# Optimization experiments

Hardware: AMD Instinct MI355X
Metric: run time of the kernel (lower is better)

The kernel has to match this reference:

```python
import jax, jax.numpy as jnp
import numpy as np

NUM_AGENTS = 4
ACTOR_DIM = 128
OBS_DIM = 64
ACTION_SIZE = 16
BATCH = 65536


def _linear_params(key, din, dout):
    kw, kb = jax.random.split(key)
    bound = 1.0 / np.sqrt(din)
    W = jax.random.uniform(kw, (din, dout), jnp.float32, -bound, bound)
    b = jax.random.uniform(kb, (dout,), jnp.float32, -bound, bound)
    return W, b


def setup_inputs() -> dict:
    key = jax.random.key(0)
    ks = jax.random.split(key, 8)
    O = jax.random.normal(ks[0], (BATCH, NUM_AGENTS, OBS_DIM), jnp.float32)
    enc_w, enc_b = _linear_params(ks[1], OBS_DIM, ACTOR_DIM)
    fc1_w, fc1_b = _linear_params(ks[2], ACTOR_DIM, ACTOR_DIM)
    fc2_w, fc2_b = _linear_params(ks[3], ACTOR_DIM, ACTOR_DIM)
    fc3_w, fc3_b = _linear_params(ks[4], ACTOR_DIM, ACTOR_DIM)
    cl4_w, cl4_b = _linear_params(ks[5], 2 * ACTOR_DIM, ACTOR_DIM)
    dec_w, dec_b = _linear_params(ks[6], NUM_AGENTS * ACTOR_DIM, ACTION_SIZE)
    return {
        "O": O,
        "enc_w": enc_w, "enc_b": enc_b,
        "fc1_w": fc1_w, "fc1_b": fc1_b,
        "fc2_w": fc2_w, "fc2_b": fc2_b,
        "fc3_w": fc3_w, "fc3_b": fc3_b,
        "cl4_w": cl4_w, "cl4_b": cl4_b,
        "dec_w": dec_w, "dec_b": dec_b,
    }


def reference(O, enc_w, enc_b, fc1_w, fc1_b, fc2_w, fc2_b, fc3_w, fc3_b,
              cl4_w, cl4_b, dec_w, dec_b):
    # Encoding: sigmoid(Linear(obs)) -> [B, A, D]
    H0 = jax.nn.sigmoid(O @ enc_w + enc_b)
    H1 = jax.nn.relu(H0 @ fc1_w + fc1_b)
    H2 = jax.nn.relu(H1 @ fc2_w + fc2_b)
    H3 = jax.nn.relu(H2 @ fc3_w + fc3_b)
    # get_commvar: masked mean over OTHER agents, but torch divides by
    # num_agents (self slot is zeroed then included in the mean).
    # Equivalent fused form: C[b,i] = (sum_j H[b,j] - H[b,i]) / num_agents
    C = (jnp.sum(H3, axis=1, keepdims=True) - H3) / NUM_AGENTS
    H_cat = jnp.concatenate([H3, C], axis=-1)          # [B, A, 2D]
    H4 = H_cat @ cl4_w + cl4_b                          # [B, A, D] (no activation)
    H = H4.reshape(-1, NUM_AGENTS * ACTOR_DIM)          # [B, A*D]
    logits = H @ dec_w + dec_b                          # [B, action_size]
    return jax.nn.softmax(logits, axis=-1)
```

## Files before the change

### kernel.cpp

```cpp
#include <hip/hip_runtime.h>
#include <stdint.h>


typedef __attribute__((ext_vector_type(4)))  float f32x4;
typedef __attribute__((ext_vector_type(16))) float f32x16;
typedef __attribute__((ext_vector_type(8)))  _Float16 f16x8;
typedef __attribute__((ext_vector_type(4)))  _Float16 f16x4;

#define WS_HALF 106496
#define SEG_ENC 0
#define SEG_FC1 8192
#define SEG_FC2 24576
#define SEG_FC3 40960
#define SEG_W1  57344
#define SEG_W2  73728
#define SEG_DEC 90112

#define MFMA16(a, b, c) __builtin_amdgcn_mfma_f32_32x32x16_f16((a), (b), (c), 0, 0, 0)

__device__ __forceinline__ unsigned short f16_bits(float f) {
  union { _Float16 h; unsigned short u; } cv;
  cv.h = (_Float16)f;
  return cv.u;
}
__device__ __forceinline__ f32x16 zero16() {
  f32x16 v;
#pragma unroll
  for (int i = 0; i < 16; ++i) v[i] = 0.0f;
  return v;
}
__device__ __forceinline__ int xswz(int row, int g) {
  return row * 128 + ((g ^ (row & 15)) << 3);
}
__device__ __forceinline__ void barrier_lds() {
  asm volatile("s_waitcnt lgkmcnt(0)\n\ts_barrier" ::: "memory");
}

__global__ void prep_weights(const float* __restrict__ enc_w, const float* __restrict__ fc1_w,
                             const float* __restrict__ fc2_w, const float* __restrict__ fc3_w,
                             const float* __restrict__ cl4_w, const float* __restrict__ dec_w,
                             unsigned short* __restrict__ ws) {
  int idx = blockIdx.x * 256 + threadIdx.x;
  if (idx >= WS_HALF) return;
  const float* W; int base, N, nbN, mode;
  if      (idx <  8192) { W = enc_w; base = SEG_ENC; N = 128; nbN = 4; mode = 0; }
  else if (idx < 24576) { W = fc1_w; base = SEG_FC1; N = 128; nbN = 4; mode = 0; }
  else if (idx < 40960) { W = fc2_w; base = SEG_FC2; N = 128; nbN = 4; mode = 0; }
  else if (idx < 57344) { W = fc3_w; base = SEG_FC3; N = 128; nbN = 4; mode = 0; }
  else if (idx < 73728) { W = cl4_w; base = SEG_W1;  N = 128; nbN = 4; mode = 1; }
  else if (idx < 90112) { W = cl4_w; base = SEG_W2;  N = 128; nbN = 4; mode = 2; }
  else                  { W = dec_w; base = SEG_DEC; N = 16;  nbN = 1; mode = 0; }
  int local = idx - base;
  int j    = local & 7;
  int lane = (local >> 3) & 63;
  int frag = local >> 9;
  int nb = frag % nbN;
  int kc = frag / nbN;
  int k = kc * 16 + ((lane >> 5) << 3) + j;
  int n = nb * 32 + (lane & 31);
  float wv;
  if (mode == 0)      wv = (n < N) ? W[k * N + n] : 0.0f;
  else if (mode == 1) wv = W[k * 128 + n] - 0.25f * W[(k + 128) * 128 + n];
  else                wv = 0.25f * W[(k + 128) * 128 + n];
  ws[idx] = f16_bits(wv);
}

template <int KC, int ACT>
__device__ __forceinline__ void layer_std(short* __restrict__ Xh,
                                          const unsigned short* __restrict__ wseg,
                                          const float* __restrict__ bias,
                                          int lr, int lh, int w) {
  const int l = lh * 32 + lr;
  f32x16 acc0 = zero16(), acc1 = zero16();
  const unsigned short* bp = wseg + w * 512 + l * 8;
  f16x8 Bh[3];
  Bh[0] = *(const f16x8*)(bp);
  if (KC > 1) Bh[1] = *(const f16x8*)(bp + 2048);
  f32x4 bv[4];
#pragma unroll
  for (int q = 0; q < 4; ++q)
    bv[q] = *(const f32x4*)&bias[w * 32 + q * 8 + 4 * lh];
  barrier_lds();
#pragma unroll
  for (int kc = 0; kc < KC; ++kc) {
    const int cur = kc % 3;
    if (kc + 2 < KC) {
      Bh[(kc + 2) % 3] = *(const f16x8*)(bp + (kc + 2) * 2048);
    }
    const int g = kc * 2 + lh;
    const int xi0 = xswz(lr, g), xi1 = xswz(lr + 32, g);
    const f16x8 ah0 = *(const f16x8*)&Xh[xi0];
    const f16x8 ah1 = *(const f16x8*)&Xh[xi1];
    acc0 = MFMA16(Bh[cur], ah0, acc0);
    acc1 = MFMA16(Bh[cur], ah1, acc1);
  }
  barrier_lds();
#pragma unroll
  for (int mb = 0; mb < 2; ++mb) {
    const int row = mb * 32 + lr;
    const int rb = row & 15;
    const f32x16 a = mb ? acc1 : acc0;
#pragma unroll
    for (int q = 0; q < 4; ++q) {
      f16x4 hq;
#pragma unroll
      for (int t = 0; t < 4; ++t) {
        float v = a[q * 4 + t] + bv[q][t];
        if (ACT == 0)      v = __builtin_amdgcn_rcpf(1.0f + __expf(-v));
        else if (ACT == 1) v = fmaxf(v, 0.0f);
        hq[t] = (_Float16)v;
      }
      const int idx = row * 128 + (((w * 4 + q) ^ rb) << 3) + 4 * lh;
      *(f16x4*)&Xh[idx] = hq;
    }
  }
}

template <int MB>
__device__ __forceinline__ f32x16 cl4_band(const short* __restrict__ Xh,
                                           const unsigned short* __restrict__ ws,
                                           const float* __restrict__ cl4_b,
                                           int lr, int lh, int w) {
  const int l = lh * 32 + lr;
  f32x16 a1 = zero16(), a2 = zero16();
  const unsigned short* b1p = ws + SEG_W1 + w * 512 + l * 8;
  const unsigned short* b2p = ws + SEG_W2 + w * 512 + l * 8;
  f16x8 B1[2], B2[2];
  B1[0] = *(const f16x8*)(b1p);
  B2[0] = *(const f16x8*)(b2p);
  f32x4 bv[4];
#pragma unroll
  for (int q = 0; q < 4; ++q)
    bv[q] = *(const f32x4*)&cl4_b[w * 32 + q * 8 + 4 * lh];
#pragma unroll
  for (int kc = 0; kc < 8; ++kc) {
    const int cur = kc & 1;
    if (kc < 7) {
      const int nx = cur ^ 1;
      B1[nx] = *(const f16x8*)(b1p + (kc + 1) * 2048);
      B2[nx] = *(const f16x8*)(b2p + (kc + 1) * 2048);
    }
    const int xi = xswz(MB * 32 + lr, kc * 2 + lh);
    const f16x8 ah = *(const f16x8*)&Xh[xi];
    a1 = MFMA16(B1[cur], ah, a1);
    a2 = MFMA16(B2[cur], ah, a2);
  }
  f32x16 res;
#pragma unroll
  for (int r = 0; r < 16; ++r) {
    float t2 = a2[r];
    t2 += __shfl_xor(t2, 1);
    t2 += __shfl_xor(t2, 2);
    res[r] = a1[r] + t2 + bv[r >> 2][r & 3];
  }
  return res;
}

template <int MB>
__device__ __forceinline__ void cl4_write(short* __restrict__ Xh,
                                          const f32x16& rs, int lr, int lh, int w) {
  const int row = MB * 32 + lr;
  const int rb = row & 15;
#pragma unroll
  for (int q = 0; q < 4; ++q) {
    f16x4 hq;
#pragma unroll
    for (int t = 0; t < 4; ++t) hq[t] = (_Float16)rs[q * 4 + t];
    const int idx = row * 128 + (((w * 4 + q) ^ rb) << 3) + 4 * lh;
    *(f16x4*)&Xh[idx] = hq;
  }
}

__global__ __launch_bounds__(256, 4)
void commnet_fwd(const float* __restrict__ O,
                 const float* __restrict__ enc_b, const float* __restrict__ fc1_b,
                 const float* __restrict__ fc2_b, const float* __restrict__ fc3_b,
                 const float* __restrict__ cl4_b, const float* __restrict__ dec_b,
                 const unsigned short* __restrict__ ws, float* __restrict__ out) {
  __shared__ __attribute__((aligned(16))) short Xh[64 * 128];
  __shared__ __attribute__((aligned(16))) float Pbuf[272];

  const int tid = threadIdx.x;
  const int l = tid & 63, w = tid >> 6;
  const int lr = l & 31, lh = l >> 5;

  Pbuf[tid] = 0.0f;
  if (tid < 16) Pbuf[256 + tid] = 0.0f;

  {
    const f32x4* Og = (const f32x4*)(O + (long)blockIdx.x * 4096);
#pragma unroll
    for (int it = 0; it < 4; ++it) {
      const int i = it * 256 + tid;
      const int row = i >> 4;
      const int c4 = (i & 15) << 2;
      f32x4 v = Og[i];
      f16x4 hv;
#pragma unroll
      for (int j = 0; j < 4; ++j) hv[j] = (_Float16)v[j];
      const int bi = row * 128 + (((c4 >> 3) ^ (row & 15)) << 3) + (c4 & 7);
      *(f16x4*)&Xh[bi] = hv;
    }
  }

  layer_std<4, 0>(Xh, ws + SEG_ENC, enc_b, lr, lh, w);
  layer_std<8, 1>(Xh, ws + SEG_FC1, fc1_b, lr, lh, w);
  layer_std<8, 1>(Xh, ws + SEG_FC2, fc2_b, lr, lh, w);
  layer_std<8, 1>(Xh, ws + SEG_FC3, fc3_b, lr, lh, w);

  barrier_lds();
  {
    const f32x16 res0 = cl4_band<0>(Xh, ws, cl4_b, lr, lh, w);
    barrier_lds();
    cl4_write<0>(Xh, res0, lr, lh, w);
  }
  {
    const f32x16 res1 = cl4_band<1>(Xh, ws, cl4_b, lr, lh, w);
    barrier_lds();
    cl4_write<1>(Xh, res1, lr, lh, w);
  }
  barrier_lds();

  {
    f32x16 dacc = zero16();
    const unsigned short* bp = ws + SEG_DEC + (w * 8) * 512 + l * 8;
    f16x8 Bh[2];
    Bh[0] = *(const f16x8*)(bp);
#pragma unroll
    for (int kq = 0; kq < 8; ++kq) {
      const int cur = kq & 1;
      if (kq < 7) {
        Bh[cur ^ 1] = *(const f16x8*)(bp + (kq + 1) * 512);
      }
      const int kcg = w * 8 + kq;
      const int k0 = kcg * 16 + lh * 8;
      const int agent = k0 >> 7;
      const int d0 = k0 & 127;
      const int row = (lr & 15) * 4 + agent;
      const int xi = xswz(row, d0 >> 3);
      const f16x8 ah = *(const f16x8*)&Xh[xi];
      dacc = MFMA16(Bh[cur], ah, dacc);
    }
    if (lr < 16) {
#pragma unroll
      for (int r = 0; r < 8; ++r) {
        const int action = (r & 3) + 8 * (r >> 2) + 4 * lh;
        atomicAdd(&Pbuf[lr * 17 + action], dacc[r]);
      }
    }
  }
  barrier_lds();

  {
    const int c = tid & 15;
    float v = Pbuf[(tid >> 4) * 17 + c] + dec_b[c];
    float m = v;
#pragma unroll
    for (int mk = 1; mk < 16; mk <<= 1) m = fmaxf(m, __shfl_xor(m, mk, 16));
    const float e = __expf(v - m);
    float s = e;
#pragma unroll
    for (int mk = 1; mk < 16; mk <<= 1) s += __shfl_xor(s, mk, 16);
    out[(long)blockIdx.x * 256 + tid] = e * __builtin_amdgcn_rcpf(s);
  }
}

extern "C" void kernel_launch(void* const* d_in, const int* in_sizes, int n_in,
                              void* d_out, int out_size, void* d_ws, size_t ws_size,
                              hipStream_t stream) {
  (void)n_in; (void)out_size; (void)ws_size;
  const float* O     = (const float*)d_in[0];
  const float* enc_w = (const float*)d_in[1];
  const float* enc_b = (const float*)d_in[2];
  const float* fc1_w = (const float*)d_in[3];
  const float* fc1_b = (const float*)d_in[4];
  const float* fc2_w = (const float*)d_in[5];
  const float* fc2_b = (const float*)d_in[6];
  const float* fc3_w = (const float*)d_in[7];
  const float* fc3_b = (const float*)d_in[8];
  const float* cl4_w = (const float*)d_in[9];
  const float* cl4_b = (const float*)d_in[10];
  const float* dec_w = (const float*)d_in[11];
  const float* dec_b = (const float*)d_in[12];
  unsigned short* wsb = (unsigned short*)d_ws;

  prep_weights<<<(WS_HALF + 255) / 256, 256, 0, stream>>>(enc_w, fc1_w, fc2_w, fc3_w,
                                                          cl4_w, dec_w, wsb);
  const int rows   = in_sizes[0] / 64;
  const int blocks = rows / 64;
  commnet_fwd<<<blocks, 256, 0, stream>>>(O, enc_b, fc1_b, fc2_b, fc3_b, cl4_b,
                                          dec_b, wsb, (float*)d_out);
}
```

Baseline: 97.09 us.

## Ping-pong LDS activation buffers and prefetch all layer weights up front

Replaces the single in-place LDS activation tile with two ping-pong buffers. Each layer now needs one barrier instead of two, and the cl4 bands no longer need barriers between the compute and write-back steps. Weight fragments for each layer (and 4-deep for cl4, all 8 for the decoder) are loaded into registers before the MFMA loop, replacing the rolling 2-3 deep prefetch. The second buffer doubles LDS use to about 33 KB per block and raises VGPR pressure, which could cost occupancy against the launch bound of 4 blocks.

```diff
diff --git a/kernel.cpp b/kernel.cpp
--- a/kernel.cpp
+++ b/kernel.cpp
@@ -66,35 +66,30 @@
 }
 
 template <int KC, int ACT>
-__device__ __forceinline__ void layer_std(short* __restrict__ Xh,
+__device__ __forceinline__ void layer_std(const short* __restrict__ Xsrc,
+                                          short* __restrict__ Xdst,
                                           const unsigned short* __restrict__ wseg,
                                           const float* __restrict__ bias,
                                           int lr, int lh, int w) {
   const int l = lh * 32 + lr;
-  f32x16 acc0 = zero16(), acc1 = zero16();
   const unsigned short* bp = wseg + w * 512 + l * 8;
-  f16x8 Bh[3];
-  Bh[0] = *(const f16x8*)(bp);
-  if (KC > 1) Bh[1] = *(const f16x8*)(bp + 2048);
+  f16x8 Bh[KC];
+#pragma unroll
+  for (int kc = 0; kc < KC; ++kc) Bh[kc] = *(const f16x8*)(bp + kc * 2048);
   f32x4 bv[4];
 #pragma unroll
   for (int q = 0; q < 4; ++q)
     bv[q] = *(const f32x4*)&bias[w * 32 + q * 8 + 4 * lh];
-  barrier_lds();
+  f32x16 acc0 = zero16(), acc1 = zero16();
 #pragma unroll
   for (int kc = 0; kc < KC; ++kc) {
-    const int cur = kc % 3;
-    if (kc + 2 < KC) {
-      Bh[(kc + 2) % 3] = *(const f16x8*)(bp + (kc + 2) * 2048);
-    }
     const int g = kc * 2 + lh;
     const int xi0 = xswz(lr, g), xi1 = xswz(lr + 32, g);
-    const f16x8 ah0 = *(const f16x8*)&Xh[xi0];
-    const f16x8 ah1 = *(const f16x8*)&Xh[xi1];
-    acc0 = MFMA16(Bh[cur], ah0, acc0);
-    acc1 = MFMA16(Bh[cur], ah1, acc1);
-  }
-  barrier_lds();
+    const f16x8 ah0 = *(const f16x8*)&Xsrc[xi0];
+    const f16x8 ah1 = *(const f16x8*)&Xsrc[xi1];
+    acc0 = MFMA16(Bh[kc], ah0, acc0);
+    acc1 = MFMA16(Bh[kc], ah1, acc1);
+  }
 #pragma unroll
   for (int mb = 0; mb < 2; ++mb) {
     const int row = mb * 32 + lr;
@@ -111,63 +106,58 @@
         hq[t] = (_Float16)v;
       }
       const int idx = row * 128 + (((w * 4 + q) ^ rb) << 3) + 4 * lh;
-      *(f16x4*)&Xh[idx] = hq;
+      *(f16x4*)&Xdst[idx] = hq;
     }
   }
 }
 
 template <int MB>
-__device__ __forceinline__ f32x16 cl4_band(const short* __restrict__ Xh,
-                                           const unsigned short* __restrict__ ws,
-                                           const float* __restrict__ cl4_b,
-                                           int lr, int lh, int w) {
+__device__ __forceinline__ void cl4_band(const short* __restrict__ Xsrc,
+                                         short* __restrict__ Xdst,
+                                         const unsigned short* __restrict__ ws,
+                                         const float* __restrict__ cl4_b,
+                                         int lr, int lh, int w) {
   const int l = lh * 32 + lr;
-  f32x16 a1 = zero16(), a2 = zero16();
   const unsigned short* b1p = ws + SEG_W1 + w * 512 + l * 8;
   const unsigned short* b2p = ws + SEG_W2 + w * 512 + l * 8;
-  f16x8 B1[2], B2[2];
-  B1[0] = *(const f16x8*)(b1p);
-  B2[0] = *(const f16x8*)(b2p);
+  f16x8 B1[4], B2[4];
+#pragma unroll
+  for (int k = 0; k < 4; ++k) {
+    B1[k] = *(const f16x8*)(b1p + k * 2048);
+    B2[k] = *(const f16x8*)(b2p + k * 2048);
+  }
   f32x4 bv[4];
 #pragma unroll
   for (int q = 0; q < 4; ++q)
     bv[q] = *(const f32x4*)&cl4_b[w * 32 + q * 8 + 4 * lh];
+  f32x16 a1 = zero16(), a2 = zero16();
 #pragma unroll
   for (int kc = 0; kc < 8; ++kc) {
-    const int cur = kc & 1;
-    if (kc < 7) {
-      const int nx = cur ^ 1;
-      B1[nx] = *(const f16x8*)(b1p + (kc + 1) * 2048);
-      B2[nx] = *(const f16x8*)(b2p + (kc + 1) * 2048);
-    }
+    const int cur = kc & 3;
     const int xi = xswz(MB * 32 + lr, kc * 2 + lh);
-    const f16x8 ah = *(const f16x8*)&Xh[xi];
+    const f16x8 ah = *(const f16x8*)&Xsrc[xi];
     a1 = MFMA16(B1[cur], ah, a1);
     a2 = MFMA16(B2[cur], ah, a2);
-  }
-  f32x16 res;
-#pragma unroll
-  for (int r = 0; r < 16; ++r) {
-    float t2 = a2[r];
-    t2 += __shfl_xor(t2, 1);
-    t2 += __shfl_xor(t2, 2);
-    res[r] = a1[r] + t2 + bv[r >> 2][r & 3];
-  }
-  return res;
-}
-
-template <int MB>
-__device__ __forceinline__ void cl4_write(short* __restrict__ Xh,
-                                          const f32x16& rs, int lr, int lh, int w) {
+    if (kc + 4 < 8) {
+      B1[cur] = *(const f16x8*)(b1p + (kc + 4) * 2048);
+      B2[cur] = *(const f16x8*)(b2p + (kc + 4) * 2048);
+    }
+  }
   const int row = MB * 32 + lr;
   const int rb = row & 15;
 #pragma unroll
   for (int q = 0; q < 4; ++q) {
     f16x4 hq;
 #pragma unroll
-    for (int t = 0; t < 4; ++t) hq[t] = (_Float16)rs[q * 4 + t];
+    for (int t = 0; t < 4; ++t) {
+      const int r = q * 4 + t;
+      float t2 = a2[r];
+      t2 += __shfl_xor(t2, 1);
+      t2 += __shfl_xor(t2, 2);
+      hq[t] = (_Float16)(a1[r] + t2 + bv[q][t]);
+    }
     const int idx = row * 128 + (((w * 4 + q) ^ rb) << 3) + 4 * lh;
-    *(f16x4*)&Xh[idx] = hq;
+    *(f16x4*)&Xdst[idx] = hq;
   }
 }
 
@@ -177,7 +167,8 @@
                  const float* __restrict__ fc2_b, const float* __restrict__ fc3_b,
                  const float* __restrict__ cl4_b, const float* __restrict__ dec_b,
                  const unsigned short* __restrict__ ws, float* __restrict__ out) {
-  __shared__ __attribute__((aligned(16))) short Xh[64 * 128];
+  __shared__ __attribute__((aligned(16))) short X0[64 * 128];
+  __shared__ __attribute__((aligned(16))) short X1[64 * 128];
   __shared__ __attribute__((aligned(16))) float Pbuf[272];
 
   const int tid = threadIdx.x;
@@ -199,47 +190,40 @@
 #pragma unroll
       for (int j = 0; j < 4; ++j) hv[j] = (_Float16)v[j];
       const int bi = row * 128 + (((c4 >> 3) ^ (row & 15)) << 3) + (c4 & 7);
-      *(f16x4*)&Xh[bi] = hv;
-    }
-  }
-
-  layer_std<4, 0>(Xh, ws + SEG_ENC, enc_b, lr, lh, w);
-  layer_std<8, 1>(Xh, ws + SEG_FC1, fc1_b, lr, lh, w);
-  layer_std<8, 1>(Xh, ws + SEG_FC2, fc2_b, lr, lh, w);
-  layer_std<8, 1>(Xh, ws + SEG_FC3, fc3_b, lr, lh, w);
-
-  barrier_lds();
+      *(f16x4*)&X0[bi] = hv;
+    }
+  }
+  barrier_lds();
+
+  layer_std<4, 0>(X0, X1, ws + SEG_ENC, enc_b, lr, lh, w);
+  barrier_lds();
+  layer_std<8, 1>(X1, X0, ws + SEG_FC1, fc1_b, lr, lh, w);
+  barrier_lds();
+  layer_std<8, 1>(X0, X1, ws + SEG_FC2, fc2_b, lr, lh, w);
+  barrier_lds();
+  layer_std<8, 1>(X1, X0, ws + SEG_FC3, fc3_b, lr, lh, w);
+  barrier_lds();
+
+  cl4_band<0>(X0, X1, ws, cl4_b, lr, lh, w);
+  cl4_band<1>(X0, X1, ws, cl4_b, lr, lh, w);
+  barrier_lds();
+
   {
-    const f32x16 res0 = cl4_band<0>(Xh, ws, cl4_b, lr, lh, w);
-    barrier_lds();
-    cl4_write<0>(Xh, res0, lr, lh, w);
-  }
-  {
-    const f32x16 res1 = cl4_band<1>(Xh, ws, cl4_b, lr, lh, w);
-    barrier_lds();
-    cl4_write<1>(Xh, res1, lr, lh, w);
-  }
-  barrier_lds();
-
-  {
+    const unsigned short* bp = ws + SEG_DEC + (w * 8) * 512 + l * 8;
+    f16x8 Bh[8];
+#pragma unroll
+    for (int kq = 0; kq < 8; ++kq) Bh[kq] = *(const f16x8*)(bp + kq * 512);
     f32x16 dacc = zero16();
-    const unsigned short* bp = ws + SEG_DEC + (w * 8) * 512 + l * 8;
-    f16x8 Bh[2];
-    Bh[0] = *(const f16x8*)(bp);
 #pragma unroll
     for (int kq = 0; kq < 8; ++kq) {
-      const int cur = kq & 1;
-      if (kq < 7) {
-        Bh[cur ^ 1] = *(const f16x8*)(bp + (kq + 1) * 512);
-      }
       const int kcg = w * 8 + kq;
       const int k0 = kcg * 16 + lh * 8;
       const int agent = k0 >> 7;
       const int d0 = k0 & 127;
       const int row = (lr & 15) * 4 + agent;
       const int xi = xswz(row, d0 >> 3);
-      const f16x8 ah = *(const f16x8*)&Xh[xi];
-      dacc = MFMA16(Bh[cur], ah, dacc);
+      const f16x8 ah = *(const f16x8*)&X1[xi];
+      dacc = MFMA16(Bh[kq], ah, dacc);
     }
     if (lr < 16) {
 #pragma unroll
```

New measurement: 89.35 us. -8.0%, faster.
